# Kernel optimization log

Hardware: AMD Instinct MI355X
Metric: run time of the kernel (lower is better)

Reference implementation:

```python
import jax, jax.numpy as jnp
import numpy as np

N_NODES = 100000
N_EDGES = 1600000
DIM = 64
NUM_HEADS = 4
HEAD_DIM = DIM // NUM_HEADS
QK_SCALE = HEAD_DIM ** -0.5
EPS = 1e-16  # matches torch_geometric softmax denominator eps


def setup_inputs() -> dict:
    key = jax.random.key(0)
    k1, k2, k3 = jax.random.split(key, 3)
    x = jax.random.normal(k1, (N_NODES, DIM), dtype=jnp.float32)
    W_qkv = jax.random.normal(k2, (DIM, 3 * DIM), dtype=jnp.float32) * (DIM ** -0.5)
    b_qkv = jnp.zeros((3 * DIM,), dtype=jnp.float32)
    edge_index = jax.random.randint(k3, (2, N_EDGES), 0, N_NODES, dtype=jnp.int64)
    return {"x": x, "W_qkv": W_qkv, "b_qkv": b_qkv, "edge_index": edge_index}


def reference(x, W_qkv, b_qkv, edge_index):
    N = x.shape[0]
    E = edge_index.shape[1]
    # qkv projection: (N, 3, H, d)
    qkv = (x @ W_qkv + b_qkv).reshape(N, 3, NUM_HEADS, HEAD_DIM)
    s = edge_index[0]  # query (source) node per edge
    t = edge_index[1]  # key/value (target) node per edge
    q = qkv[s, 0] * QK_SCALE  # (E, H, d)
    k = qkv[t, 1]             # (E, H, d)
    v = qkv[t, 2]             # (E, H, d)
    compat = jnp.einsum('ehd,ehd->eh', q, k)  # (E, H)
    # segment softmax keyed by source node (numerically stable)
    m = jax.ops.segment_max(compat, s, num_segments=N)          # (N, H)
    ex = jnp.exp(compat - m[s])                                  # (E, H)
    den = jax.ops.segment_sum(ex, s, num_segments=N)             # (N, H)
    attn = ex / (den[s] + EPS)                                   # (E, H)
    # weighted values, flatten heads, scatter-sum back to source nodes
    msg = (v * attn[..., None]).reshape(E, DIM)                  # (E, dim)
    out = jax.ops.segment_sum(msg, s, num_segments=N)            # (N, dim)
    return out
```

## Files before the change

### kernel.cpp

```cpp
#include <hip/hip_runtime.h>

constexpr int N_NODES = 100000;
constexpr int N_EDGES = 1600000;
constexpr int DIM = 64;
constexpr float QK_SCALE = 0.25f;
constexpr float LOG2E = 1.4426950408889634f;
constexpr float EPS = 1e-16f;

constexpr int NBK = (N_NODES + 255) / 256;
constexpr int BCAP = 8192;
constexpr int SC_CHUNK = 8192;
constexpr int SC_THREADS = 512;
constexpr int SC_BLOCKS = (N_EDGES + SC_CHUNK - 1) / SC_CHUNK;

typedef __attribute__((ext_vector_type(8))) short short8;
typedef __attribute__((ext_vector_type(4))) float f32x4;

__device__ __forceinline__ unsigned short f32_to_bf16_rne(float f) {
    unsigned int u = __float_as_uint(f);
    u += 0x7fffu + ((u >> 16) & 1u);
    return (unsigned short)(u >> 16);
}
__device__ __forceinline__ float bf_lo(unsigned int u) { return __uint_as_float(u << 16); }
__device__ __forceinline__ float bf_hi(unsigned int u) { return __uint_as_float(u & 0xffff0000u); }

__device__ __forceinline__ float qsum4(float p) {
    int a = __builtin_amdgcn_update_dpp(0, __float_as_int(p), 0xB1, 0xF, 0xF, true);
    p += __int_as_float(a);
    int c = __builtin_amdgcn_update_dpp(0, __float_as_int(p), 0x4E, 0xF, 0xF, true);
    p += __int_as_float(c);
    return p;
}

__device__ __forceinline__ int orig_col(int jp) {
    if (jp < 64) return jp;
    const int p = jp - 64;
    const int chunk = p >> 3, w = p & 7;
    return (w < 4) ? (64 + chunk * 4 + w) : (128 + chunk * 4 + (w - 4));
}

__global__ __launch_bounds__(192) void prep_w(const float* __restrict__ W,
                                              const float* __restrict__ b,
                                              unsigned short* __restrict__ Wbt,
                                              float* __restrict__ bb,
                                              int* __restrict__ bcnt) {
    const int jp = threadIdx.x;
    const int k = blockIdx.x;
    const int oc = orig_col(jp);
    const float sc = (jp < 64) ? QK_SCALE * LOG2E : 1.f;
    Wbt[jp * DIM + k] = f32_to_bf16_rne(W[k * 192 + oc] * sc);
    if (k == 0) {
        bb[jp] = b[oc] * sc;
        for (int i = jp; i < NBK; i += 192) bcnt[i] = 0;
    }
}

__global__ __launch_bounds__(256) void qkv_mfma(const float* __restrict__ x,
                                                const unsigned short* __restrict__ Wbt,
                                                const float* __restrict__ bb,
                                                unsigned short* __restrict__ qkv_t) {
    const int lane = threadIdx.x & 63;
    const int wid = threadIdx.x >> 6;
    const int n0 = blockIdx.x * 64 + wid * 16;
    if (n0 >= N_NODES) return;
    const int row = lane & 15;
    const int kg = lane >> 4;

    const int nidx = min(n0 + row, N_NODES - 1);
    const float* xr = x + (size_t)nidx * DIM + kg * 8;
    short8 a0, a1;
    {
        const float4 u0 = *(const float4*)(xr);
        const float4 u1 = *(const float4*)(xr + 4);
        const float4 u2 = *(const float4*)(xr + 32);
        const float4 u3 = *(const float4*)(xr + 36);
        a0[0] = (short)f32_to_bf16_rne(u0.x); a0[1] = (short)f32_to_bf16_rne(u0.y);
        a0[2] = (short)f32_to_bf16_rne(u0.z); a0[3] = (short)f32_to_bf16_rne(u0.w);
        a0[4] = (short)f32_to_bf16_rne(u1.x); a0[5] = (short)f32_to_bf16_rne(u1.y);
        a0[6] = (short)f32_to_bf16_rne(u1.z); a0[7] = (short)f32_to_bf16_rne(u1.w);
        a1[0] = (short)f32_to_bf16_rne(u2.x); a1[1] = (short)f32_to_bf16_rne(u2.y);
        a1[2] = (short)f32_to_bf16_rne(u2.z); a1[3] = (short)f32_to_bf16_rne(u2.w);
        a1[4] = (short)f32_to_bf16_rne(u3.x); a1[5] = (short)f32_to_bf16_rne(u3.y);
        a1[6] = (short)f32_to_bf16_rne(u3.z); a1[7] = (short)f32_to_bf16_rne(u3.w);
    }

    #pragma unroll
    for (int ct = 0; ct < 12; ++ct) {
        const int c0 = ct * 16;
        const float bias = bb[c0 + row];
        f32x4 acc = {bias, bias, bias, bias};
        const short8 b0 = *(const short8*)(Wbt + (c0 + row) * DIM + kg * 8);
        const short8 b1 = *(const short8*)(Wbt + (c0 + row) * DIM + kg * 8 + 32);
        acc = __builtin_amdgcn_mfma_f32_16x16x32_bf16(a0, b0, acc, 0, 0, 0);
        acc = __builtin_amdgcn_mfma_f32_16x16x32_bf16(a1, b1, acc, 0, 0, 0);

        const int colg = c0 + row;
        #pragma unroll
        for (int r = 0; r < 4; ++r) {
            const int node = n0 + kg * 4 + r;
            if (node < N_NODES)
                qkv_t[(size_t)node * 192 + colg] = f32_to_bf16_rne(acc[r]);
        }
    }
}

__global__ __launch_bounds__(SC_THREADS) void bucket_scatter(const int* __restrict__ ei,
                                                             int* __restrict__ bcnt,
                                                             unsigned int* __restrict__ bbuf) {
    __shared__ int h[NBK];
    __shared__ int lofs[NBK];
    __shared__ int gbase[NBK];
    __shared__ int wsum[SC_THREADS / 64];
    __shared__ unsigned int stage[SC_CHUNK];

    const int tid = threadIdx.x;
    const int lane = tid & 63;
    const int wid = tid >> 6;
    const int e0 = blockIdx.x * SC_CHUNK;
    const int n = min(SC_CHUNK, N_EDGES - e0);

    for (int i = tid; i < NBK; i += SC_THREADS) h[i] = 0;
    __syncthreads();

    for (int i = tid; i < n; i += SC_THREADS)
        atomicAdd(&h[ei[e0 + i] >> 8], 1);
    __syncthreads();

    const int v = (tid < NBK) ? h[tid] : 0;
    int inc = v;
    #pragma unroll
    for (int d = 1; d < 64; d <<= 1) {
        int u = __shfl_up(inc, d);
        if (lane >= d) inc += u;
    }
    if (lane == 63) wsum[wid] = inc;
    __syncthreads();
    int woff = 0;
    for (int w = 0; w < wid; ++w) woff += wsum[w];
    if (tid < NBK) lofs[tid] = woff + inc - v;
    if (tid < NBK) gbase[tid] = (v > 0) ? atomicAdd(&bcnt[tid], v) : 0;
    __syncthreads();

    for (int i = tid; i < NBK; i += SC_THREADS) h[i] = 0;
    __syncthreads();

    for (int i = tid; i < n; i += SC_THREADS) {
        const int s = ei[e0 + i];
        const int t = ei[N_EDGES + e0 + i];
        const int bk = s >> 8;
        const int c = atomicAdd(&h[bk], 1);
        stage[lofs[bk] + c] = (unsigned int)t | ((unsigned int)(s & 255) << 17);
    }
    __syncthreads();

    for (int bk = wid; bk < NBK; bk += SC_THREADS / 64) {
        const int cnt = h[bk];
        const int lo = lofs[bk];
        unsigned int* dst = bbuf + (size_t)bk * BCAP + gbase[bk];
        for (int i = lane; i < cnt; i += 64) dst[i] = stage[lo + i];
    }
}

__global__ __launch_bounds__(256) void csr_build(const int* __restrict__ bcnt,
                                                 const unsigned int* __restrict__ bbuf,
                                                 int* __restrict__ deg,
                                                 int* __restrict__ off,
                                                 int* __restrict__ sorted_t) {
    __shared__ int h[256];
    __shared__ int lofs[256];
    __shared__ int wsum[4];
    __shared__ int sBase;

    const int tid = threadIdx.x;
    const int lane = tid & 63;
    const int wid = tid >> 6;
    const int bk = blockIdx.x;
    const int n = bcnt[bk];

    int pre = 0;
    for (int i = tid; i < bk; i += 256) pre += bcnt[i];
    #pragma unroll
    for (int d = 1; d < 64; d <<= 1) pre += __shfl_xor(pre, d);
    if (lane == 0) wsum[wid] = pre;
    h[tid] = 0;
    __syncthreads();
    if (tid == 0) sBase = wsum[0] + wsum[1] + wsum[2] + wsum[3];
    __syncthreads();

    const unsigned int* p = bbuf + (size_t)bk * BCAP;
    for (int i = tid; i < n; i += 256)
        atomicAdd(&h[p[i] >> 17], 1);
    __syncthreads();

    const int v = h[tid];
    int inc = v;
    #pragma unroll
    for (int d = 1; d < 64; d <<= 1) {
        int u = __shfl_up(inc, d);
        if (lane >= d) inc += u;
    }
    if (lane == 63) wsum[wid] = inc;
    __syncthreads();
    int woff = 0;
    for (int w = 0; w < wid; ++w) woff += wsum[w];
    const int exc = woff + inc - v;
    lofs[tid] = exc;
    const int node = bk * 256 + tid;
    if (node < N_NODES) { deg[node] = v; off[node] = sBase + exc; }
    __syncthreads();

    h[tid] = 0;
    __syncthreads();
    int* dstbase = sorted_t + sBase;
    for (int i = tid; i < n; i += 256) {
        const unsigned int e = p[i];
        const int s8 = e >> 17;
        const int c = atomicAdd(&h[s8], 1);
        dstbase[lofs[s8] + c] = (int)(e & 0x1FFFFu);
    }
}

__global__ __launch_bounds__(256) void node_pass(const unsigned short* __restrict__ qkv,
                                                 const int* __restrict__ off,
                                                 const int* __restrict__ deg,
                                                 const int* __restrict__ sorted_t,
                                                 float* __restrict__ out) {
    const int node = blockIdx.x * 4 + (threadIdx.x >> 6);
    const int lane = threadIdx.x & 63;
    if (node >= N_NODES) return;
    const int eg = lane >> 4;
    const int q16 = lane & 15;

    const int o = off[node];
    const int d = deg[node];

    const uint2 qu = *(const uint2*)(qkv + (size_t)node * 192 + q16 * 4);
    const float qx = bf_lo(qu.x), qy = bf_hi(qu.x);
    const float qz = bf_lo(qu.y), qw = bf_hi(qu.y);

    const float NEG_INF = -__builtin_inff();
    float m = NEG_INF;
    float l = 0.f;
    float4 acc = make_float4(0.f, 0.f, 0.f, 0.f);

    for (int base = 0; base < d; base += 64) {
        const int nb = min(64, d - base);
        int tb = (base + lane < d) ? sorted_t[o + base + lane] : 0;
        for (int j16 = 0; j16 < nb; j16 += 16) {
            const int i0 = j16 + eg;
            const int t0 = __shfl(tb, i0);
            const int t1 = __shfl(tb, i0 + 4);
            const int t2 = __shfl(tb, i0 + 8);
            const int t3 = __shfl(tb, i0 + 12);
            const uint4 A0 = *(const uint4*)(qkv + (size_t)t0 * 192 + 64 + q16 * 8);
            const uint4 A1 = *(const uint4*)(qkv + (size_t)t1 * 192 + 64 + q16 * 8);
            const uint4 A2 = *(const uint4*)(qkv + (size_t)t2 * 192 + 64 + q16 * 8);
            const uint4 A3 = *(const uint4*)(qkv + (size_t)t3 * 192 + 64 + q16 * 8);
            float p0 = qx * bf_lo(A0.x) + qy * bf_hi(A0.x) + qz * bf_lo(A0.y) + qw * bf_hi(A0.y);
            float p1 = qx * bf_lo(A1.x) + qy * bf_hi(A1.x) + qz * bf_lo(A1.y) + qw * bf_hi(A1.y);
            float p2 = qx * bf_lo(A2.x) + qy * bf_hi(A2.x) + qz * bf_lo(A2.y) + qw * bf_hi(A2.y);
            float p3 = qx * bf_lo(A3.x) + qy * bf_hi(A3.x) + qz * bf_lo(A3.y) + qw * bf_hi(A3.y);
            p0 = qsum4(p0); p1 = qsum4(p1); p2 = qsum4(p2); p3 = qsum4(p3);
            p0 = (i0      < nb) ? p0 : NEG_INF;
            p1 = (i0 + 4  < nb) ? p1 : NEG_INF;
            p2 = (i0 + 8  < nb) ? p2 : NEG_INF;
            p3 = (i0 + 12 < nb) ? p3 : NEG_INF;
            float pm = fmaxf(fmaxf(p0, p1), fmaxf(p2, p3));
            pm = fmaxf(pm, __shfl_xor(pm, 16));
            pm = fmaxf(pm, __shfl_xor(pm, 32));
            if (__any(pm > m)) {
                const float nm = fmaxf(m, pm);
                const float sc = exp2f(m - nm);
                l *= sc;
                acc.x *= sc; acc.y *= sc; acc.z *= sc; acc.w *= sc;
                m = nm;
            }
            const float e0 = exp2f(p0 - m);
            const float e1 = exp2f(p1 - m);
            const float e2 = exp2f(p2 - m);
            const float e3 = exp2f(p3 - m);
            l += (e0 + e1) + (e2 + e3);
            acc.x = fmaf(e0, bf_lo(A0.z), fmaf(e1, bf_lo(A1.z),
                    fmaf(e2, bf_lo(A2.z), fmaf(e3, bf_lo(A3.z), acc.x))));
            acc.y = fmaf(e0, bf_hi(A0.z), fmaf(e1, bf_hi(A1.z),
                    fmaf(e2, bf_hi(A2.z), fmaf(e3, bf_hi(A3.z), acc.y))));
            acc.z = fmaf(e0, bf_lo(A0.w), fmaf(e1, bf_lo(A1.w),
                    fmaf(e2, bf_lo(A2.w), fmaf(e3, bf_lo(A3.w), acc.z))));
            acc.w = fmaf(e0, bf_hi(A0.w), fmaf(e1, bf_hi(A1.w),
                    fmaf(e2, bf_hi(A2.w), fmaf(e3, bf_hi(A3.w), acc.w))));
        }
    }
    l += __shfl_xor(l, 16);  l += __shfl_xor(l, 32);
    acc.x += __shfl_xor(acc.x, 16);  acc.x += __shfl_xor(acc.x, 32);
    acc.y += __shfl_xor(acc.y, 16);  acc.y += __shfl_xor(acc.y, 32);
    acc.z += __shfl_xor(acc.z, 16);  acc.z += __shfl_xor(acc.z, 32);
    acc.w += __shfl_xor(acc.w, 16);  acc.w += __shfl_xor(acc.w, 32);

    if (eg == 0) {
        const float inv = 1.f / (l + EPS);
        float4 r = make_float4(acc.x * inv, acc.y * inv, acc.z * inv, acc.w * inv);
        *(float4*)(out + (size_t)node * DIM + q16 * 4) = r;
    }
}

extern "C" void kernel_launch(void* const* d_in, const int* in_sizes, int n_in,
                              void* d_out, int out_size, void* d_ws, size_t ws_size,
                              hipStream_t stream) {
    const float* x = (const float*)d_in[0];
    const float* W = (const float*)d_in[1];
    const float* b = (const float*)d_in[2];
    const int*   ei = (const int*)d_in[3];
    float* out = (float*)d_out;

    unsigned short* qkv_t = (unsigned short*)d_ws;
    unsigned int* bbuf = (unsigned int*)(qkv_t + (size_t)N_NODES * 192);
    int* sorted_t = (int*)(bbuf + (size_t)NBK * BCAP);
    int* deg      = sorted_t + N_EDGES;
    int* off      = deg + N_NODES;
    int* bcnt     = off + N_NODES;
    unsigned short* Wbt = (unsigned short*)(bcnt + NBK);
    float* bb     = (float*)(Wbt + 192 * DIM);

    prep_w<<<64, 192, 0, stream>>>(W, b, Wbt, bb, bcnt);
    qkv_mfma<<<(N_NODES + 63) / 64, 256, 0, stream>>>(x, Wbt, bb, qkv_t);
    bucket_scatter<<<SC_BLOCKS, SC_THREADS, 0, stream>>>(ei, bcnt, bbuf);
    csr_build<<<NBK, 256, 0, stream>>>(bcnt, bbuf, deg, off, sorted_t);
    node_pass<<<(N_NODES + 3) / 4, 256, 0, stream>>>(qkv_t, off, deg, sorted_t, out);
}
```

Before: 135.1 us.

## Merge QKV projection with edge bucket scatter and use per-lane online softmax

```diff
diff --git a/kernel.cpp b/kernel.cpp
--- a/kernel.cpp
+++ b/kernel.cpp
@@ -10,8 +10,8 @@
 constexpr int NBK = (N_NODES + 255) / 256;
 constexpr int BCAP = 8192;
 constexpr int SC_CHUNK = 8192;
-constexpr int SC_THREADS = 512;
 constexpr int SC_BLOCKS = (N_EDGES + SC_CHUNK - 1) / SC_CHUNK;
+constexpr int QK_BLOCKS = (N_NODES + 127) / 128;
 
 typedef __attribute__((ext_vector_type(8))) short short8;
 typedef __attribute__((ext_vector_type(4))) float f32x4;
@@ -55,109 +55,110 @@
     }
 }
 
-__global__ __launch_bounds__(256) void qkv_mfma(const float* __restrict__ x,
-                                                const unsigned short* __restrict__ Wbt,
-                                                const float* __restrict__ bb,
-                                                unsigned short* __restrict__ qkv_t) {
-    const int lane = threadIdx.x & 63;
-    const int wid = threadIdx.x >> 6;
-    const int n0 = blockIdx.x * 64 + wid * 16;
-    if (n0 >= N_NODES) return;
-    const int row = lane & 15;
-    const int kg = lane >> 4;
-
-    const int nidx = min(n0 + row, N_NODES - 1);
-    const float* xr = x + (size_t)nidx * DIM + kg * 8;
-    short8 a0, a1;
-    {
-        const float4 u0 = *(const float4*)(xr);
-        const float4 u1 = *(const float4*)(xr + 4);
-        const float4 u2 = *(const float4*)(xr + 32);
-        const float4 u3 = *(const float4*)(xr + 36);
-        a0[0] = (short)f32_to_bf16_rne(u0.x); a0[1] = (short)f32_to_bf16_rne(u0.y);
-        a0[2] = (short)f32_to_bf16_rne(u0.z); a0[3] = (short)f32_to_bf16_rne(u0.w);
-        a0[4] = (short)f32_to_bf16_rne(u1.x); a0[5] = (short)f32_to_bf16_rne(u1.y);
-        a0[6] = (short)f32_to_bf16_rne(u1.z); a0[7] = (short)f32_to_bf16_rne(u1.w);
-        a1[0] = (short)f32_to_bf16_rne(u2.x); a1[1] = (short)f32_to_bf16_rne(u2.y);
-        a1[2] = (short)f32_to_bf16_rne(u2.z); a1[3] = (short)f32_to_bf16_rne(u2.w);
-        a1[4] = (short)f32_to_bf16_rne(u3.x); a1[5] = (short)f32_to_bf16_rne(u3.y);
-        a1[6] = (short)f32_to_bf16_rne(u3.z); a1[7] = (short)f32_to_bf16_rne(u3.w);
-    }
-
-    #pragma unroll
-    for (int ct = 0; ct < 12; ++ct) {
-        const int c0 = ct * 16;
-        const float bias = bb[c0 + row];
-        f32x4 acc = {bias, bias, bias, bias};
-        const short8 b0 = *(const short8*)(Wbt + (c0 + row) * DIM + kg * 8);
-        const short8 b1 = *(const short8*)(Wbt + (c0 + row) * DIM + kg * 8 + 32);
-        acc = __builtin_amdgcn_mfma_f32_16x16x32_bf16(a0, b0, acc, 0, 0, 0);
-        acc = __builtin_amdgcn_mfma_f32_16x16x32_bf16(a1, b1, acc, 0, 0, 0);
-
-        const int colg = c0 + row;
-        #pragma unroll
-        for (int r = 0; r < 4; ++r) {
-            const int node = n0 + kg * 4 + r;
-            if (node < N_NODES)
-                qkv_t[(size_t)node * 192 + colg] = f32_to_bf16_rne(acc[r]);
-        }
-    }
-}
-
-__global__ __launch_bounds__(SC_THREADS) void bucket_scatter(const int* __restrict__ ei,
-                                                             int* __restrict__ bcnt,
-                                                             unsigned int* __restrict__ bbuf) {
+__global__ __launch_bounds__(512) void proj_scatter(const float* __restrict__ x,
+                                                    const unsigned short* __restrict__ Wbt,
+                                                    const float* __restrict__ bb,
+                                                    unsigned short* __restrict__ qkv_t,
+                                                    const int* __restrict__ ei,
+                                                    int* __restrict__ bcnt,
+                                                    unsigned int* __restrict__ bbuf) {
     __shared__ int h[NBK];
     __shared__ int lofs[NBK];
     __shared__ int gbase[NBK];
-    __shared__ int wsum[SC_THREADS / 64];
+    __shared__ int wsum[8];
     __shared__ unsigned int stage[SC_CHUNK];
 
-    const int tid = threadIdx.x;
-    const int lane = tid & 63;
-    const int wid = tid >> 6;
-    const int e0 = blockIdx.x * SC_CHUNK;
-    const int n = min(SC_CHUNK, N_EDGES - e0);
-
-    for (int i = tid; i < NBK; i += SC_THREADS) h[i] = 0;
-    __syncthreads();
-
-    for (int i = tid; i < n; i += SC_THREADS)
-        atomicAdd(&h[ei[e0 + i] >> 8], 1);
-    __syncthreads();
-
-    const int v = (tid < NBK) ? h[tid] : 0;
-    int inc = v;
-    #pragma unroll
-    for (int d = 1; d < 64; d <<= 1) {
-        int u = __shfl_up(inc, d);
-        if (lane >= d) inc += u;
-    }
-    if (lane == 63) wsum[wid] = inc;
-    __syncthreads();
-    int woff = 0;
-    for (int w = 0; w < wid; ++w) woff += wsum[w];
-    if (tid < NBK) lofs[tid] = woff + inc - v;
-    if (tid < NBK) gbase[tid] = (v > 0) ? atomicAdd(&bcnt[tid], v) : 0;
-    __syncthreads();
-
-    for (int i = tid; i < NBK; i += SC_THREADS) h[i] = 0;
-    __syncthreads();
-
-    for (int i = tid; i < n; i += SC_THREADS) {
-        const int s = ei[e0 + i];
-        const int t = ei[N_EDGES + e0 + i];
-        const int bk = s >> 8;
-        const int c = atomicAdd(&h[bk], 1);
-        stage[lofs[bk] + c] = (unsigned int)t | ((unsigned int)(s & 255) << 17);
-    }
-    __syncthreads();
-
-    for (int bk = wid; bk < NBK; bk += SC_THREADS / 64) {
-        const int cnt = h[bk];
-        const int lo = lofs[bk];
-        unsigned int* dst = bbuf + (size_t)bk * BCAP + gbase[bk];
-        for (int i = lane; i < cnt; i += 64) dst[i] = stage[lo + i];
+    if (blockIdx.x < SC_BLOCKS) {
+        const int tid = threadIdx.x;
+        const int lane = tid & 63;
+        const int wid = tid >> 6;
+        const int e0 = blockIdx.x * SC_CHUNK;
+        const int n = min(SC_CHUNK, N_EDGES - e0);
+
+        for (int i = tid; i < NBK; i += 512) h[i] = 0;
+        __syncthreads();
+
+        for (int i = tid; i < n; i += 512)
+            atomicAdd(&h[ei[e0 + i] >> 8], 1);
+        __syncthreads();
+
+        const int v = (tid < NBK) ? h[tid] : 0;
+        int inc = v;
+        #pragma unroll
+        for (int d = 1; d < 64; d <<= 1) {
+            int u = __shfl_up(inc, d);
+            if (lane >= d) inc += u;
+        }
+        if (lane == 63) wsum[wid] = inc;
+        __syncthreads();
+        int woff = 0;
+        for (int w = 0; w < wid; ++w) woff += wsum[w];
+        if (tid < NBK) lofs[tid] = woff + inc - v;
+        if (tid < NBK) gbase[tid] = (v > 0) ? atomicAdd(&bcnt[tid], v) : 0;
+        __syncthreads();
+
+        for (int i = tid; i < NBK; i += 512) h[i] = 0;
+        __syncthreads();
+
+        for (int i = tid; i < n; i += 512) {
+            const int s = ei[e0 + i];
+            const int t = ei[N_EDGES + e0 + i];
+            const int bk = s >> 8;
+            const int c = atomicAdd(&h[bk], 1);
+            stage[lofs[bk] + c] = (unsigned int)t | ((unsigned int)(s & 255) << 17);
+        }
+        __syncthreads();
+
+        for (int bk = wid; bk < NBK; bk += 8) {
+            const int cnt = h[bk];
+            const int lo = lofs[bk];
+            unsigned int* dst = bbuf + (size_t)bk * BCAP + gbase[bk];
+            for (int i = lane; i < cnt; i += 64) dst[i] = stage[lo + i];
+        }
+    } else {
+        const int lane = threadIdx.x & 63;
+        const int wid = threadIdx.x >> 6;
+        const int n0 = (blockIdx.x - SC_BLOCKS) * 128 + wid * 16;
+        if (n0 >= N_NODES) return;
+        const int row = lane & 15;
+        const int kg = lane >> 4;
+
+        const int nidx = min(n0 + row, N_NODES - 1);
+        const float* xr = x + (size_t)nidx * DIM + kg * 8;
+        short8 a0, a1;
+        {
+            const float4 u0 = *(const float4*)(xr);
+            const float4 u1 = *(const float4*)(xr + 4);
+            const float4 u2 = *(const float4*)(xr + 32);
+            const float4 u3 = *(const float4*)(xr + 36);
+            a0[0] = (short)f32_to_bf16_rne(u0.x); a0[1] = (short)f32_to_bf16_rne(u0.y);
+            a0[2] = (short)f32_to_bf16_rne(u0.z); a0[3] = (short)f32_to_bf16_rne(u0.w);
+            a0[4] = (short)f32_to_bf16_rne(u1.x); a0[5] = (short)f32_to_bf16_rne(u1.y);
+            a0[6] = (short)f32_to_bf16_rne(u1.z); a0[7] = (short)f32_to_bf16_rne(u1.w);
+            a1[0] = (short)f32_to_bf16_rne(u2.x); a1[1] = (short)f32_to_bf16_rne(u2.y);
+            a1[2] = (short)f32_to_bf16_rne(u2.z); a1[3] = (short)f32_to_bf16_rne(u2.w);
+            a1[4] = (short)f32_to_bf16_rne(u3.x); a1[5] = (short)f32_to_bf16_rne(u3.y);
+            a1[6] = (short)f32_to_bf16_rne(u3.z); a1[7] = (short)f32_to_bf16_rne(u3.w);
+        }
+
+        #pragma unroll
+        for (int ct = 0; ct < 12; ++ct) {
+            const int c0 = ct * 16;
+            const float bias = bb[c0 + row];
+            f32x4 acc = {bias, bias, bias, bias};
+            const short8 b0 = *(const short8*)(Wbt + (c0 + row) * DIM + kg * 8);
+            const short8 b1 = *(const short8*)(Wbt + (c0 + row) * DIM + kg * 8 + 32);
+            acc = __builtin_amdgcn_mfma_f32_16x16x32_bf16(a0, b0, acc, 0, 0, 0);
+            acc = __builtin_amdgcn_mfma_f32_16x16x32_bf16(a1, b1, acc, 0, 0, 0);
+
+            const int colg = c0 + row;
+            #pragma unroll
+            for (int r = 0; r < 4; ++r) {
+                const int node = n0 + kg * 4 + r;
+                if (node < N_NODES)
+                    qkv_t[(size_t)node * 192 + colg] = f32_to_bf16_rne(acc[r]);
+            }
+        }
     }
 }
 
@@ -238,58 +239,60 @@
     const float qx = bf_lo(qu.x), qy = bf_hi(qu.x);
     const float qz = bf_lo(qu.y), qw = bf_hi(qu.y);
 
-    const float NEG_INF = -__builtin_inff();
-    float m = NEG_INF;
+    const float M0 = -1e30f, MASKV = -2e30f;
+    float m = M0;
     float l = 0.f;
     float4 acc = make_float4(0.f, 0.f, 0.f, 0.f);
 
-    for (int base = 0; base < d; base += 64) {
-        const int nb = min(64, d - base);
-        int tb = (base + lane < d) ? sorted_t[o + base + lane] : 0;
-        for (int j16 = 0; j16 < nb; j16 += 16) {
-            const int i0 = j16 + eg;
-            const int t0 = __shfl(tb, i0);
-            const int t1 = __shfl(tb, i0 + 4);
-            const int t2 = __shfl(tb, i0 + 8);
-            const int t3 = __shfl(tb, i0 + 12);
-            const uint4 A0 = *(const uint4*)(qkv + (size_t)t0 * 192 + 64 + q16 * 8);
-            const uint4 A1 = *(const uint4*)(qkv + (size_t)t1 * 192 + 64 + q16 * 8);
-            const uint4 A2 = *(const uint4*)(qkv + (size_t)t2 * 192 + 64 + q16 * 8);
-            const uint4 A3 = *(const uint4*)(qkv + (size_t)t3 * 192 + 64 + q16 * 8);
-            float p0 = qx * bf_lo(A0.x) + qy * bf_hi(A0.x) + qz * bf_lo(A0.y) + qw * bf_hi(A0.y);
-            float p1 = qx * bf_lo(A1.x) + qy * bf_hi(A1.x) + qz * bf_lo(A1.y) + qw * bf_hi(A1.y);
-            float p2 = qx * bf_lo(A2.x) + qy * bf_hi(A2.x) + qz * bf_lo(A2.y) + qw * bf_hi(A2.y);
-            float p3 = qx * bf_lo(A3.x) + qy * bf_hi(A3.x) + qz * bf_lo(A3.y) + qw * bf_hi(A3.y);
-            p0 = qsum4(p0); p1 = qsum4(p1); p2 = qsum4(p2); p3 = qsum4(p3);
-            p0 = (i0      < nb) ? p0 : NEG_INF;
-            p1 = (i0 + 4  < nb) ? p1 : NEG_INF;
-            p2 = (i0 + 8  < nb) ? p2 : NEG_INF;
-            p3 = (i0 + 12 < nb) ? p3 : NEG_INF;
-            float pm = fmaxf(fmaxf(p0, p1), fmaxf(p2, p3));
-            pm = fmaxf(pm, __shfl_xor(pm, 16));
-            pm = fmaxf(pm, __shfl_xor(pm, 32));
-            if (__any(pm > m)) {
-                const float nm = fmaxf(m, pm);
-                const float sc = exp2f(m - nm);
-                l *= sc;
-                acc.x *= sc; acc.y *= sc; acc.z *= sc; acc.w *= sc;
-                m = nm;
-            }
-            const float e0 = exp2f(p0 - m);
-            const float e1 = exp2f(p1 - m);
-            const float e2 = exp2f(p2 - m);
-            const float e3 = exp2f(p3 - m);
-            l += (e0 + e1) + (e2 + e3);
-            acc.x = fmaf(e0, bf_lo(A0.z), fmaf(e1, bf_lo(A1.z),
-                    fmaf(e2, bf_lo(A2.z), fmaf(e3, bf_lo(A3.z), acc.x))));
-            acc.y = fmaf(e0, bf_hi(A0.z), fmaf(e1, bf_hi(A1.z),
-                    fmaf(e2, bf_hi(A2.z), fmaf(e3, bf_hi(A3.z), acc.y))));
-            acc.z = fmaf(e0, bf_lo(A0.w), fmaf(e1, bf_lo(A1.w),
-                    fmaf(e2, bf_lo(A2.w), fmaf(e3, bf_lo(A3.w), acc.z))));
-            acc.w = fmaf(e0, bf_hi(A0.w), fmaf(e1, bf_hi(A1.w),
-                    fmaf(e2, bf_hi(A2.w), fmaf(e3, bf_hi(A3.w), acc.w))));
-        }
-    }
+    for (int j = 0; j < d; j += 16) {
+        const int b0 = j + eg * 4;
+        const int dm = d - 1;
+        const int t0 = sorted_t[o + min(b0,     dm)];
+        const int t1 = sorted_t[o + min(b0 + 1, dm)];
+        const int t2 = sorted_t[o + min(b0 + 2, dm)];
+        const int t3 = sorted_t[o + min(b0 + 3, dm)];
+        const uint4 A0 = *(const uint4*)(qkv + (size_t)t0 * 192 + 64 + q16 * 8);
+        const uint4 A1 = *(const uint4*)(qkv + (size_t)t1 * 192 + 64 + q16 * 8);
+        const uint4 A2 = *(const uint4*)(qkv + (size_t)t2 * 192 + 64 + q16 * 8);
+        const uint4 A3 = *(const uint4*)(qkv + (size_t)t3 * 192 + 64 + q16 * 8);
+        float p0 = qx * bf_lo(A0.x) + qy * bf_hi(A0.x) + qz * bf_lo(A0.y) + qw * bf_hi(A0.y);
+        float p1 = qx * bf_lo(A1.x) + qy * bf_hi(A1.x) + qz * bf_lo(A1.y) + qw * bf_hi(A1.y);
+        float p2 = qx * bf_lo(A2.x) + qy * bf_hi(A2.x) + qz * bf_lo(A2.y) + qw * bf_hi(A2.y);
+        float p3 = qx * bf_lo(A3.x) + qy * bf_hi(A3.x) + qz * bf_lo(A3.y) + qw * bf_hi(A3.y);
+        p0 = qsum4(p0); p1 = qsum4(p1); p2 = qsum4(p2); p3 = qsum4(p3);
+        p0 = (b0     < d) ? p0 : MASKV;
+        p1 = (b0 + 1 < d) ? p1 : MASKV;
+        p2 = (b0 + 2 < d) ? p2 : MASKV;
+        p3 = (b0 + 3 < d) ? p3 : MASKV;
+        const float pm = fmaxf(fmaxf(p0, p1), fmaxf(p2, p3));
+        if (__any(pm > m)) {
+            const float nm = fmaxf(m, pm);
+            const float sc = exp2f(m - nm);
+            l *= sc;
+            acc.x *= sc; acc.y *= sc; acc.z *= sc; acc.w *= sc;
+            m = nm;
+        }
+        const float e0 = exp2f(p0 - m);
+        const float e1 = exp2f(p1 - m);
+        const float e2 = exp2f(p2 - m);
+        const float e3 = exp2f(p3 - m);
+        l += (e0 + e1) + (e2 + e3);
+        acc.x = fmaf(e0, bf_lo(A0.z), fmaf(e1, bf_lo(A1.z),
+                fmaf(e2, bf_lo(A2.z), fmaf(e3, bf_lo(A3.z), acc.x))));
+        acc.y = fmaf(e0, bf_hi(A0.z), fmaf(e1, bf_hi(A1.z),
+                fmaf(e2, bf_hi(A2.z), fmaf(e3, bf_hi(A3.z), acc.y))));
+        acc.z = fmaf(e0, bf_lo(A0.w), fmaf(e1, bf_lo(A1.w),
+                fmaf(e2, bf_lo(A2.w), fmaf(e3, bf_lo(A3.w), acc.z))));
+        acc.w = fmaf(e0, bf_hi(A0.w), fmaf(e1, bf_hi(A1.w),
+                fmaf(e2, bf_hi(A2.w), fmaf(e3, bf_hi(A3.w), acc.w))));
+    }
+
+    float M = fmaxf(m, __shfl_xor(m, 16));
+    M = fmaxf(M, __shfl_xor(M, 32));
+    const float s = exp2f(m - M);
+    l *= s;
+    acc.x *= s; acc.y *= s; acc.z *= s; acc.w *= s;
+
     l += __shfl_xor(l, 16);  l += __shfl_xor(l, 32);
     acc.x += __shfl_xor(acc.x, 16);  acc.x += __shfl_xor(acc.x, 32);
     acc.y += __shfl_xor(acc.y, 16);  acc.y += __shfl_xor(acc.y, 32);
@@ -322,8 +325,7 @@
     float* bb     = (float*)(Wbt + 192 * DIM);
 
     prep_w<<<64, 192, 0, stream>>>(W, b, Wbt, bb, bcnt);
-    qkv_mfma<<<(N_NODES + 63) / 64, 256, 0, stream>>>(x, Wbt, bb, qkv_t);
-    bucket_scatter<<<SC_BLOCKS, SC_THREADS, 0, stream>>>(ei, bcnt, bbuf);
+    proj_scatter<<<SC_BLOCKS + QK_BLOCKS, 512, 0, stream>>>(x, Wbt, bb, qkv_t, ei, bcnt, bbuf);
     csr_build<<<NBK, 256, 0, stream>>>(bcnt, bbuf, deg, off, sorted_t);
     node_pass<<<(N_NODES + 3) / 4, 256, 0, stream>>>(qkv_t, off, deg, sorted_t, out);
 }
```

After: 128.7 us. 4.8% less time.
